# Kernel tuning notes

Hardware: AMD Instinct MI355X
Metric: run time of the kernel (lower is better)

## Reference

```python
import jax, jax.numpy as jnp
import numpy as np

B, IN, ED, PW, OUT, CL, NK = 2048, 4096, 8192, 2048, 256, 16, 32
MIX = 0.5

def _onehot_mask(key, n):
    # near-one-hot selector matrix [n, NK], as built by forward_update_masks
    idx = jax.random.choice(key, n, (NK,), replace=False)
    return jnp.zeros((n, NK), jnp.float32).at[idx, jnp.arange(NK)].set(1.0)

def setup_inputs():
    ks = jax.random.split(jax.random.key(0), 24)
    f = jnp.float32
    adj = (jax.random.uniform(ks[4], (IN, IN)) < 0.01).astype(f)
    adj = jnp.maximum(adj, adj.T).at[jnp.arange(IN), jnp.arange(IN)].set(1.0)
    return {
        'x_gene': jax.random.normal(ks[0], (B, IN), f),
        'x_invmea': jax.random.normal(ks[1], (B, IN), f),
        'x_curv': jax.random.normal(ks[2], (B, ED), f),
        'clinn': jax.random.normal(ks[3], (B, CL), f),
        'Adj': adj,
        'edge_mask': (jax.random.uniform(ks[5], (ED, IN)) < 0.005).astype(f),
        'pathway_mask': (jax.random.uniform(ks[6], (PW, ED)) < 0.02).astype(f),
        'top_gene_mask': _onehot_mask(ks[7], IN),
        'top_invmea_mask': _onehot_mask(ks[8], IN),
        'top_curv_mask': _onehot_mask(ks[9], ED),
        'top_path_mask': _onehot_mask(ks[10], PW),
        'W1': jnp.full((IN, IN), 0.05, f),
        'b1': 0.01 * jax.random.normal(ks[11], (IN,), f),
        'W2': jnp.full((ED, IN), 0.05, f),
        'b2': 0.01 * jax.random.normal(ks[12], (ED,), f),
        'W3': jnp.full((PW, ED), 0.05, f),
        'b3': 0.01 * jax.random.normal(ks[13], (PW,), f),
        'W4': 0.02 * jax.random.normal(ks[14], (OUT, PW), f),
        'b4': 0.01 * jax.random.normal(ks[15], (OUT,), f),
        'W5': 0.02 * jax.random.normal(ks[16], (OUT, OUT), f),
        'b5': 0.01 * jax.random.normal(ks[17], (OUT,), f),
        'W6': 0.05 * jax.random.normal(ks[18], (OUT, OUT + CL + 4 * NK), f),
        'W7': 0.05 * jax.random.normal(ks[19], (1, OUT), f),
        'mp11': MIX * jnp.ones(IN, f),
        'mp12': (1.0 - MIX) * jnp.ones(IN, f),
        'mp1': jnp.ones(IN, f),
        'mp21': MIX * jnp.ones(ED, f),
        'mp22': (1.0 - MIX) * jnp.ones(ED, f),
        'mp2': jnp.ones(ED, f),
        'mp3': jnp.ones(PW, f),
    }

def reference(x_gene, x_invmea, x_curv, clinn, Adj, edge_mask, pathway_mask,
              top_gene_mask, top_invmea_mask, top_curv_mask, top_path_mask,
              W1, b1, W2, b2, W3, b3, W4, b4, W5, b5, W6, W7,
              mp11, mp12, mp1, mp21, mp22, mp2, mp3):
    sg = jax.lax.stop_gradient
    sig = jax.nn.sigmoid
    kept_gene = sg(x_gene @ top_gene_mask)                     # [B,NK] gather-as-matmul
    x1 = sig(x_gene @ (W1 * Adj).T + b1)                       # masked linear [B,IN]
    x1 = x_invmea * (mp11 * mp1) + x1 * (mp12 * mp1)
    kept_invmea = sg(x1 @ top_invmea_mask)
    x1 = sig(x1 @ (W2 * edge_mask).T + b2)                     # [B,ED]
    x1 = x_curv * (mp21 * mp2) + x1 * (mp22 * mp2)
    kept_curv = sg(x1 @ top_curv_mask)
    x1 = sig(x1 @ (W3 * pathway_mask).T + b3)                  # [B,PW]
    x1 = x1 * mp3
    kept_path = sg(x1 @ top_path_mask)
    x1 = sig(x1 @ W4.T + b4)
    x1 = sig(x1 @ W5.T + b5)                                   # [B,OUT]
    x_cat = jnp.concatenate([x1, kept_gene, kept_invmea, kept_curv, kept_path, clinn], axis=1)
    lp = sig(x_cat @ W6.T)
    lp = lp - jnp.mean(lp, axis=1, keepdims=True)
    return lp @ W7.T                                           # [B,1]
```

## Files before the change

kernel.cpp:

```cpp
#include <hip/hip_runtime.h>

typedef unsigned short u16;
typedef __attribute__((ext_vector_type(4))) float f32x4;
typedef __attribute__((ext_vector_type(8))) short s16x8;

__device__ __forceinline__ u16 f2bf(float f) {
    union { float f; unsigned u; } c; c.f = f;
    return (u16)((c.u + 0x7fffu + ((c.u >> 16) & 1u)) >> 16);
}
__device__ __forceinline__ float bf2f(u16 u) {
    union { unsigned u; float f; } c; c.u = ((unsigned)u) << 16; return c.f;
}
__device__ __forceinline__ unsigned pk2(float a, float b) {
    return (unsigned)f2bf(a) | ((unsigned)f2bf(b) << 16);
}
__device__ __forceinline__ float sigm(float x) { return 1.0f / (1.0f + __expf(-x)); }
__device__ __forceinline__ void fma2(unsigned xv, float w, float& a0, float& a1) {
    union { float f; unsigned u; } lo, hi;
    lo.u = xv << 16; hi.u = xv & 0xFFFF0000u;
    a0 += w * lo.f; a1 += w * hi.f;
}

__device__ __forceinline__ void load16_g2l(const void* g, void* l) {
    __builtin_amdgcn_global_load_lds(
        (const __attribute__((address_space(1))) unsigned int*)(unsigned long long)g,
        (__attribute__((address_space(3))) unsigned int*)(unsigned int)(unsigned long long)l,
        16, 0, 0);
}

#define GSTR 2112

__device__ void d_transpF(const float* __restrict__ in, u16* __restrict__ out,
                          int ldo, int Cc, int bx, int by, float (*t)[65]) {
    const int r0 = by * 64, c0 = bx * 64;
    const int tid = threadIdx.x;
#pragma unroll
    for (int i = 0; i < 4; i++) {
        int idx = tid + i * 256;
        int rr = idx >> 4, c4 = (idx & 15) * 4;
        float4 v = *(const float4*)(in + (size_t)(r0 + rr) * Cc + c0 + c4);
        t[rr][c4 + 0] = v.x; t[rr][c4 + 1] = v.y;
        t[rr][c4 + 2] = v.z; t[rr][c4 + 3] = v.w;
    }
    __syncthreads();
#pragma unroll
    for (int i = 0; i < 8; i++) {
        int idx = tid + i * 256;
        int cc = idx >> 5, rp = (idx & 31) * 2;
        unsigned p = pk2(t[rp][cc], t[rp + 1][cc]);
        *(unsigned*)(out + (size_t)(c0 + cc) * ldo + r0 + rp) = p;
    }
}

__device__ void d_find(const float* __restrict__ mask, int n, int* __restrict__ outp,
                       int* red, int k) {
    int best = -1;
    for (int i = threadIdx.x; i < n; i += 256)
        if (mask[(size_t)i * 32 + k] != 0.0f) best = i;
    red[threadIdx.x] = best;
    __syncthreads();
    for (int off = 128; off > 0; off >>= 1) {
        if (threadIdx.x < off) {
            int o = red[threadIdx.x + off];
            if (o > red[threadIdx.x]) red[threadIdx.x] = o;
        }
        __syncthreads();
    }
    if (threadIdx.x == 0) *outp = red[0] < 0 ? 0 : red[0];
}

__device__ void d_conv(const float* __restrict__ in, u16* __restrict__ out,
                       int bid, unsigned n8) {
    unsigned i = bid * 256u + threadIdx.x;
    if (i >= n8) return;
    float4 a = ((const float4*)in)[2 * i];
    float4 b = ((const float4*)in)[2 * i + 1];
    uint4 o;
    o.x = pk2(a.x, a.y); o.y = pk2(a.z, a.w);
    o.z = pk2(b.x, b.y); o.w = pk2(b.z, b.w);
    ((uint4*)out)[i] = o;
}

template <int SUBC>
__device__ void d_ell_row(const float* __restrict__ M, const float* __restrict__ W,
                          unsigned* __restrict__ ell, int* __restrict__ cnt,
                          int PAD, int row, int* __restrict__ lds) {
    const int lane = threadIdx.x & 63;
    const int wv = threadIdx.x >> 6;
    const int C = SUBC * 4096;
    const float4* mrow = (const float4*)(M + (size_t)row * C);
    const float4* wrow = (const float4*)(W + (size_t)row * C);
    unsigned* erow = ell + (size_t)row * PAD;

    float4 m[SUBC * 4];
#pragma unroll
    for (int k = 0; k < SUBC * 4; k++) {
        int sc = k >> 2, i = k & 3;
        m[k] = mrow[(wv * SUBC + sc) * 256 + lane + i * 64];
    }
    unsigned bits[SUBC];
    int total = 0;
#pragma unroll
    for (int sc = 0; sc < SUBC; sc++) {
        unsigned b = 0;
#pragma unroll
        for (int i = 0; i < 4; i++) {
            const float4 mm = m[sc * 4 + i];
            if (mm.x != 0.f) b |= 1u << (4 * i);
            if (mm.y != 0.f) b |= 2u << (4 * i);
            if (mm.z != 0.f) b |= 4u << (4 * i);
            if (mm.w != 0.f) b |= 8u << (4 * i);
        }
        bits[sc] = b;
        total += __popc(b);
    }
    float4 w[SUBC * 4];
#pragma unroll
    for (int k = 0; k < SUBC * 4; k++) {
        int sc = k >> 2, i = k & 3;
        if ((bits[sc] >> (4 * i)) & 0xFu)
            w[k] = wrow[(wv * SUBC + sc) * 256 + lane + i * 64];
    }
    int pre = total;
#pragma unroll
    for (int off = 1; off < 64; off <<= 1) {
        int t = __shfl_up(pre, off, 64);
        if (lane >= off) pre += t;
    }
    if (lane == 63) lds[wv] = pre;
    __syncthreads();
    int base = 0;
#pragma unroll
    for (int v = 0; v < 3; v++) if (v < wv) base += lds[v];
    int s = base + pre - total;
    __asm__ volatile("" ::: "memory");
#pragma unroll
    for (int sc = 0; sc < SUBC; sc++) {
        const unsigned b = bits[sc];
        const int f4b = (wv * SUBC + sc) * 256;
#pragma unroll
        for (int i = 0; i < 4; i++) {
            if ((b >> (4 * i)) & 0xFu) {
                const float4 wv4 = w[sc * 4 + i];
                int c = (f4b + lane + i * 64) * 4;
                if (b & (1u << (4 * i))) { if (s < PAD) erow[s] = ((unsigned)f2bf(wv4.x) << 16) | (unsigned)(c + 0); s++; }
                if (b & (2u << (4 * i))) { if (s < PAD) erow[s] = ((unsigned)f2bf(wv4.y) << 16) | (unsigned)(c + 1); s++; }
                if (b & (4u << (4 * i))) { if (s < PAD) erow[s] = ((unsigned)f2bf(wv4.z) << 16) | (unsigned)(c + 2); s++; }
                if (b & (8u << (4 * i))) { if (s < PAD) erow[s] = ((unsigned)f2bf(wv4.w) << 16) | (unsigned)(c + 3); s++; }
            }
        }
    }
    if (threadIdx.x == 0) {
        int rt = lds[0] + lds[1] + lds[2] + lds[3];
        cnt[row] = rt > PAD ? PAD : rt;
    }
}

__global__ __launch_bounds__(256) void prep_part(
    int ebase, int ecount, int mbase, int mcount,
    const float* __restrict__ Adj, const float* __restrict__ W1,
    unsigned* __restrict__ ell1, int* __restrict__ cnt1,
    const float* __restrict__ edge, const float* __restrict__ W2,
    unsigned* __restrict__ ell2, int* __restrict__ cnt2,
    const float* __restrict__ path, const float* __restrict__ W3,
    unsigned* __restrict__ ell3, int* __restrict__ cnt3,
    const float* __restrict__ xg_f, const float* __restrict__ xinv_f,
    const float* __restrict__ xcv_f,
    u16* __restrict__ xTg, u16* __restrict__ xinvT, u16* __restrict__ xcvT,
    const float* __restrict__ m0, const float* __restrict__ m1,
    const float* __restrict__ m2, const float* __restrict__ m3,
    int* __restrict__ idx,
    const float* __restrict__ W4, u16* __restrict__ w4b,
    const float* __restrict__ W5, u16* __restrict__ w5b) {
    __shared__ float tile[64][65];
    const long long T = ecount + mcount, E = ecount;
    const int b = blockIdx.x;
    const int ea = (int)(((long long)b * E) / T);
    const int eb2 = (int)(((long long)(b + 1) * E) / T);
    if (eb2 > ea) {
        int id = ebase + ea;
        if (id < 4096) { d_ell_row<1>(Adj, W1, ell1, cnt1, 256, id, (int*)tile); return; }
        id -= 4096;
        if (id < 8192) { d_ell_row<1>(edge, W2, ell2, cnt2, 96, id, (int*)tile); return; }
        d_ell_row<2>(path, W3, ell3, cnt3, 320, id - 8192, (int*)tile);
        return;
    }
    int id = mbase + (b - ea);
    if (id < 2048) { d_transpF(xg_f, xTg, GSTR, 4096, id & 63, id >> 6, tile); return; }
    id -= 2048;
    if (id < 2048) { d_transpF(xinv_f, xinvT, 2048, 4096, id & 63, id >> 6, tile); return; }
    id -= 2048;
    if (id < 4096) { d_transpF(xcv_f, xcvT, 2048, 8192, id & 127, id >> 7, tile); return; }
    id -= 4096;
    if (id < 128) {
        const float* mk; int n;
        int which = id >> 5;
        if (which == 0)      { mk = m0; n = 4096; }
        else if (which == 1) { mk = m1; n = 4096; }
        else if (which == 2) { mk = m2; n = 8192; }
        else                 { mk = m3; n = 2048; }
        d_find(mk, n, idx + which * 32 + (id & 31), (int*)tile, id & 31);
        return;
    }
    id -= 128;
    if (id < 256) { d_conv(W4, w4b, id, 65536u); return; }
    id -= 256;
    d_conv(W5, w5b, id, 8192u);
}

template <int BPL, int LAYER, int XSTR, int ISTR, int OSTR>
__global__ __launch_bounds__(256) void spmm(const unsigned* __restrict__ ell,
                                            const int* __restrict__ cnt,
                                            const u16* __restrict__ xT,
                                            u16* __restrict__ outT,
                                            const float* __restrict__ bias,
                                            const float* __restrict__ c1a,
                                            const float* __restrict__ c1b,
                                            const float* __restrict__ c2a,
                                            const float* __restrict__ c2b,
                                            const u16* __restrict__ invT,
                                            const int* __restrict__ gidx,
                                            u16* __restrict__ gdst,
                                            int PAD) {
    const int lane = threadIdx.x & 63;
    const int wv = __builtin_amdgcn_readfirstlane((int)(threadIdx.x >> 6));
    const int j = blockIdx.x * 4 + wv;
    const int b0 = blockIdx.y * (64 * BPL) + lane * BPL;

    const unsigned* ep = ell + (size_t)j * PAD;
    int len = cnt[j];
    if (len > PAD) len = PAD;

    float acc[BPL];
#pragma unroll
    for (int i = 0; i < BPL; i++) acc[i] = 0.f;

    const int nfull = len >> 3;
    unsigned eA[8];
    if (nfull > 0) {
#pragma unroll
        for (int t = 0; t < 8; t++) eA[t] = ep[t];
    }
    for (int g = 0; g < nfull; g++) {
        unsigned eB[8];
        const bool more = (g + 1 < nfull);
        if (more) {
#pragma unroll
            for (int t = 0; t < 8; t++) eB[t] = ep[(g + 1) * 8 + t];
        }
        uint2 xv[8];
#pragma unroll
        for (int t = 0; t < 8; t++)
            xv[t] = *(const uint2*)(xT + (size_t)(eA[t] & 0xFFFFu) * XSTR + b0);
#pragma unroll
        for (int t = 0; t < 8; t++) {
            union { float f; unsigned u; } w; w.u = (eA[t] >> 16) << 16;
            fma2(xv[t].x, w.f, acc[0], acc[1]);
            fma2(xv[t].y, w.f, acc[2], acc[3]);
        }
        if (more) {
#pragma unroll
            for (int t = 0; t < 8; t++) eA[t] = eB[t];
        }
    }
    for (int s = nfull * 8; s < len; ++s) {
        unsigned e = ep[s];
        union { float f; unsigned u; } w; w.u = (e >> 16) << 16;
        const u16* xp = xT + (size_t)(e & 0xFFFFu) * XSTR + b0;
        uint2 xv = *(const uint2*)xp;
        fma2(xv.x, w.f, acc[0], acc[1]); fma2(xv.y, w.f, acc[2], acc[3]);
    }

    const float bi = bias[j];
    float c1 = 0.f;
    if (c1a) { c1 = c1a[j]; if (c1b) c1 *= c1b[j]; }
    float c2 = 1.f;
    if (c2a) { c2 = c2a[j]; if (c2b) c2 *= c2b[j]; }

    float v[BPL];
#pragma unroll
    for (int i = 0; i < BPL; i++) v[i] = sigm(acc[i] + bi) * c2;
    if (invT) {
        const unsigned long long* ip = (const unsigned long long*)(invT + (size_t)j * ISTR + b0);
#pragma unroll
        for (int h = 0; h < BPL / 4; h++) {
            unsigned long long iv = __builtin_nontemporal_load(ip + h);
            unsigned lo = (unsigned)iv, hi = (unsigned)(iv >> 32);
            union { float f; unsigned u; } g0, g1, g2, g3;
            g0.u = lo << 16; g1.u = lo & 0xFFFF0000u;
            g2.u = hi << 16; g3.u = hi & 0xFFFF0000u;
            v[4 * h + 0] += g0.f * c1; v[4 * h + 1] += g1.f * c1;
            v[4 * h + 2] += g2.f * c1; v[4 * h + 3] += g3.f * c1;
        }
    }
    unsigned long long pkv[BPL / 4];
#pragma unroll
    for (int h = 0; h < BPL / 4; h++)
        pkv[h] = (unsigned long long)pk2(v[4 * h + 0], v[4 * h + 1])
               | ((unsigned long long)pk2(v[4 * h + 2], v[4 * h + 3]) << 32);
    unsigned long long* op = (unsigned long long*)(outT + (size_t)j * OSTR + b0);
#pragma unroll
    for (int h = 0; h < BPL / 4; h++) __builtin_nontemporal_store(pkv[h], op + h);

    if (gdst) {
        for (int t = 0; t < 32; t++) {
            if (gidx[t] == j) {
                unsigned long long* gp = (unsigned long long*)(gdst + t * 2048 + b0);
#pragma unroll
                for (int h = 0; h < BPL / 4; h++) gp[h] = pkv[h];
            }
        }
    }
}

template <int XSTR>
__global__ __launch_bounds__(256) void spmm_ph(const unsigned* __restrict__ ell,
                                               const int* __restrict__ cnt,
                                               const u16* __restrict__ xT,
                                               u16* __restrict__ outT,
                                               const float* __restrict__ bias,
                                               const float* __restrict__ scale,
                                               const int* __restrict__ gidx,
                                               u16* __restrict__ gdst,
                                               int PAD) {
    const int lane = threadIdx.x & 63;
    const int wv = __builtin_amdgcn_readfirstlane((int)(threadIdx.x >> 6));
    const int j = blockIdx.x * 4 + wv;
    const int b0 = blockIdx.y * 128 + lane * 2;

    const unsigned* ep = ell + (size_t)j * PAD;
    int len = cnt[j];
    if (len > PAD) len = PAD;

    float a0 = 0.f, a1 = 0.f;
    const int nfull = len >> 4;
    unsigned eA[16];
    if (nfull > 0) {
#pragma unroll
        for (int t = 0; t < 16; t++) eA[t] = ep[t];
    }
    for (int g = 0; g < nfull; g++) {
        unsigned eB[16];
        const bool more = (g + 1 < nfull);
        if (more) {
#pragma unroll
            for (int t = 0; t < 16; t++) eB[t] = ep[(g + 1) * 16 + t];
        }
        unsigned xv[16];
#pragma unroll
        for (int t = 0; t < 16; t++)
            xv[t] = *(const unsigned*)(xT + (size_t)(eA[t] & 0xFFFFu) * XSTR + b0);
#pragma unroll
        for (int t = 0; t < 16; t++) {
            union { float f; unsigned u; } w; w.u = (eA[t] >> 16) << 16;
            fma2(xv[t], w.f, a0, a1);
        }
        if (more) {
#pragma unroll
            for (int t = 0; t < 16; t++) eA[t] = eB[t];
        }
    }
    for (int s = nfull * 16; s < len; ++s) {
        unsigned e = ep[s];
        union { float f; unsigned u; } w; w.u = (e >> 16) << 16;
        unsigned xv = *(const unsigned*)(xT + (size_t)(e & 0xFFFFu) * XSTR + b0);
        fma2(xv, w.f, a0, a1);
    }

    const float bi = bias[j];
    const float sc = scale[j];
    const unsigned pk = pk2(sigm(a0 + bi) * sc, sigm(a1 + bi) * sc);
    *(unsigned*)(outT + ((size_t)j << 11) + b0) = pk;

    if (gdst) {
        for (int t = 0; t < 32; t++) {
            if (gidx[t] == j)
                *(unsigned*)(gdst + t * 2048 + b0) = pk;
        }
    }
}

__global__ __launch_bounds__(256) void gatherFT(const float* __restrict__ src, int ld,
                                                const int* __restrict__ idx,
                                                u16* __restrict__ dstT) {
    int i = blockIdx.x * 256 + threadIdx.x;
    int kk = i >> 11, b = i & 2047;
    dstT[i] = f2bf(src[(size_t)b * ld + idx[kk]]);
}

__global__ __launch_bounds__(256) void transpB(const u16* __restrict__ in,
                                               u16* __restrict__ out, int Rr, int Cc) {
    __shared__ u16 t[64][66];
    const int r0 = blockIdx.y * 64, c0 = blockIdx.x * 64;
    const int tid = threadIdx.x;
#pragma unroll
    for (int i = 0; i < 16; i++) {
        int idx = tid + i * 256;
        int rr = idx >> 6, cc = idx & 63;
        t[rr][cc] = in[(size_t)(r0 + rr) * Cc + c0 + cc];
    }
    __syncthreads();
#pragma unroll
    for (int i = 0; i < 16; i++) {
        int idx = tid + i * 256;
        int cc = idx >> 6, rr = idx & 63;
        out[(size_t)(c0 + cc) * Rr + r0 + rr] = t[rr][cc];
    }
}

template <int WR, int WC, int MF, int NF, int KC, int WPE>
__global__ __launch_bounds__(WR * WC * 64, WPE)
void gemm_t(const u16* __restrict__ A, const u16* __restrict__ W,
            u16* __restrict__ Out, const float* __restrict__ bias, int N, int K) {
    constexpr int NTHR = WR * WC * 64;
    constexpr int BM = WR * MF * 16;
    constexpr int BN = WC * NF * 16;
    constexpr int BK = KC * 32;
    constexpr int CPR = KC * 4;
    constexpr int MSK = CPR - 1;
    constexpr int CA = BM * CPR / NTHR;
    constexpr int CB = BN * CPR / NTHR;
    constexpr int L  = CA + CB;

    __shared__ u16 At[2][BM * BK];
    __shared__ u16 Bt[2][BN * BK];

    const int tid = threadIdx.x;
    const int lane = tid & 63;
    const int wave = tid >> 6;
    const int wr = wave / WC, wc = wave % WC;
    const int tn = blockIdx.x, tm = blockIdx.y;
    const int r16 = lane & 15;
    const int q = lane >> 4;

    const u16* aSrc[CA]; int aDst[CA];
#pragma unroll
    for (int j = 0; j < CA; j++) {
        int c = tid + j * NTHR;
        int r = c / CPR, p = c - r * CPR;
        aSrc[j] = A + (size_t)(tm * BM + r) * K + (p ^ (r & MSK)) * 8;
        aDst[j] = c * 8;
    }
    const u16* bSrc[CB]; int bDst[CB];
#pragma unroll
    for (int j = 0; j < CB; j++) {
        int c = tid + j * NTHR;
        int r = c / CPR, p = c - r * CPR;
        bSrc[j] = W + (size_t)(tn * BN + r) * K + (p ^ (r & MSK)) * 8;
        bDst[j] = c * 8;
    }
    int aRd[MF][KC], bRd[NF][KC];
#pragma unroll
    for (int mi = 0; mi < MF; mi++)
#pragma unroll
        for (int kc = 0; kc < KC; kc++)
            aRd[mi][kc] = (wr * MF * 16 + mi * 16 + r16) * BK + (((kc * 4 + q) ^ (r16 & MSK)) << 3);
#pragma unroll
    for (int ni = 0; ni < NF; ni++)
#pragma unroll
        for (int kc = 0; kc < KC; kc++)
            bRd[ni][kc] = (wc * NF * 16 + ni * 16 + r16) * BK + (((kc * 4 + q) ^ (r16 & MSK)) << 3);

    const int nIter = K / BK;

#define ISSUE(slot, it_)                                              \
    do {                                                              \
        const int k0_ = (it_) * BK;                                   \
        _Pragma("unroll")                                             \
        for (int j = 0; j < CA; j++)                                  \
            load16_g2l(aSrc[j] + k0_, &At[slot][aDst[j]]);            \
        _Pragma("unroll")                                             \
        for (int j = 0; j < CB; j++)                                  \
            load16_g2l(bSrc[j] + k0_, &Bt[slot][bDst[j]]);            \
    } while (0)

    ISSUE(0, 0);
    if (nIter > 1) ISSUE(1, 1);

    f32x4 acc[MF][NF];
#pragma unroll
    for (int i = 0; i < MF; i++)
#pragma unroll
        for (int j = 0; j < NF; j++) acc[i][j] = (f32x4){0.f, 0.f, 0.f, 0.f};

    for (int it = 0; it < nIter; ++it) {
        const int s = it & 1;
        if (it + 1 < nIter) __builtin_amdgcn_s_waitcnt(0xF70 | L);
        else                __builtin_amdgcn_s_waitcnt(0xF70);
        __asm__ volatile("" ::: "memory");
        __builtin_amdgcn_s_barrier();
        __asm__ volatile("" ::: "memory");

        s16x8 af[KC][MF], bfr[KC][NF];
#pragma unroll
        for (int kc = 0; kc < KC; kc++) {
#pragma unroll
            for (int mi = 0; mi < MF; mi++) af[kc][mi] = *(const s16x8*)(&At[s][aRd[mi][kc]]);
#pragma unroll
            for (int ni = 0; ni < NF; ni++) bfr[kc][ni] = *(const s16x8*)(&Bt[s][bRd[ni][kc]]);
        }
        __asm__ volatile("" ::: "memory");
        __builtin_amdgcn_s_waitcnt(0xC07F);
        __builtin_amdgcn_s_barrier();
        __asm__ volatile("" ::: "memory");

        if (it + 2 < nIter) ISSUE(s, it + 2);

#pragma unroll
        for (int kc = 0; kc < KC; kc++)
#pragma unroll
            for (int mi = 0; mi < MF; mi++)
#pragma unroll
                for (int ni = 0; ni < NF; ni++)
                    acc[mi][ni] = __builtin_amdgcn_mfma_f32_16x16x32_bf16(af[kc][mi], bfr[kc][ni], acc[mi][ni], 0, 0, 0);
    }
#undef ISSUE

#pragma unroll
    for (int ni = 0; ni < NF; ni++) {
        const int n = tn * BN + wc * NF * 16 + ni * 16 + r16;
        const float bi = bias ? bias[n] : 0.f;
#pragma unroll
        for (int mi = 0; mi < MF; mi++) {
#pragma unroll
            for (int rg = 0; rg < 4; rg++) {
                const int m = tm * BM + wr * MF * 16 + mi * 16 + q * 4 + rg;
                Out[(size_t)m * N + n] = f2bf(sigm(acc[mi][ni][rg] + bi));
            }
        }
    }
}

__global__ __launch_bounds__(256) void tail_k(const u16* __restrict__ x5,
                                              const u16* __restrict__ kgT,
                                              const u16* __restrict__ kiT,
                                              const u16* __restrict__ kcT,
                                              const u16* __restrict__ kpT,
                                              const float* __restrict__ clinn,
                                              const float* __restrict__ W6,
                                              const float* __restrict__ W7,
                                              float* __restrict__ out) {
    __shared__ float xs[8 * 400];
    __shared__ float s1[4][8], s2[4][8], s3[4];
    const int tid = threadIdx.x;
    const int b0 = blockIdx.x * 8;
    for (int i = tid; i < 8 * 400; i += 256) {
        int r = i / 400, c = i - r * 400;
        int b = b0 + r;
        float v;
        if (c < 256)      v = bf2f(x5[b * 256 + c]);
        else if (c < 288) v = bf2f(kgT[(c - 256) * 2048 + b]);
        else if (c < 320) v = bf2f(kiT[(c - 288) * 2048 + b]);
        else if (c < 352) v = bf2f(kcT[(c - 320) * 2048 + b]);
        else if (c < 384) v = bf2f(kpT[(c - 352) * 2048 + b]);
        else              v = clinn[b * 16 + (c - 384)];
        xs[i] = v;
    }
    __syncthreads();
    const int j = tid;
    float acc[8];
#pragma unroll
    for (int r = 0; r < 8; r++) acc[r] = 0.f;
    const float4* wrow = (const float4*)(W6 + (size_t)j * 400);
    for (int c = 0; c < 100; c++) {
        float4 wv = wrow[c];
        const float* wp = (const float*)&wv;
#pragma unroll
        for (int t = 0; t < 4; t++) {
            float w = wp[t];
            int k = c * 4 + t;
#pragma unroll
            for (int r = 0; r < 8; r++) acc[r] += w * xs[r * 400 + k];
        }
    }
    const float w7j = W7[j];
    const int lane = tid & 63, wave = tid >> 6;
    float t3 = w7j;
#pragma unroll
    for (int off = 32; off > 0; off >>= 1) t3 += __shfl_down(t3, off, 64);
    if (lane == 0) s3[wave] = t3;
#pragma unroll
    for (int r = 0; r < 8; r++) {
        float lp = sigm(acc[r]);
        float t1 = lp, t2 = lp * w7j;
#pragma unroll
        for (int off = 32; off > 0; off >>= 1) {
            t1 += __shfl_down(t1, off, 64);
            t2 += __shfl_down(t2, off, 64);
        }
        if (lane == 0) { s1[wave][r] = t1; s2[wave][r] = t2; }
    }
    __syncthreads();
    if (tid < 8) {
        float S1 = s1[0][tid] + s1[1][tid] + s1[2][tid] + s1[3][tid];
        float S2 = s2[0][tid] + s2[1][tid] + s2[2][tid] + s2[3][tid];
        float SW = s3[0] + s3[1] + s3[2] + s3[3];
        out[b0 + tid] = S2 - (S1 * (1.f / 256.f)) * SW;
    }
}

extern "C" void kernel_launch(void* const* d_in, const int* in_sizes, int n_in,
                              void* d_out, int out_size, void* d_ws, size_t ws_size,
                              hipStream_t stream) {
    const float* x_gene   = (const float*)d_in[0];
    const float* x_invmea = (const float*)d_in[1];
    const float* x_curv   = (const float*)d_in[2];
    const float* clinn    = (const float*)d_in[3];
    const float* Adj      = (const float*)d_in[4];
    const float* edge_m   = (const float*)d_in[5];
    const float* path_m   = (const float*)d_in[6];
    const float* tg_mask  = (const float*)d_in[7];
    const float* ti_mask  = (const float*)d_in[8];
    const float* tc_mask  = (const float*)d_in[9];
    const float* tp_mask  = (const float*)d_in[10];
    const float* W1 = (const float*)d_in[11];  const float* b1 = (const float*)d_in[12];
    const float* W2 = (const float*)d_in[13];  const float* b2 = (const float*)d_in[14];
    const float* W3 = (const float*)d_in[15];  const float* b3 = (const float*)d_in[16];
    const float* W4 = (const float*)d_in[17];  const float* b4 = (const float*)d_in[18];
    const float* W5 = (const float*)d_in[19];  const float* b5 = (const float*)d_in[20];
    const float* W6 = (const float*)d_in[21];
    const float* W7 = (const float*)d_in[22];
    const float* mp11 = (const float*)d_in[23];
    const float* mp12 = (const float*)d_in[24];
    const float* mp1  = (const float*)d_in[25];
    const float* mp21 = (const float*)d_in[26];
    const float* mp22 = (const float*)d_in[27];
    const float* mp2  = (const float*)d_in[28];
    const float* mp3  = (const float*)d_in[29];

    char* ws = (char*)d_ws;
    const float* nulf = nullptr;
    float* out = (float*)d_out;

    u16*  xTg   = (u16*)(ws + 0);
    u16*  x3T   = (u16*)(ws + 0);
    u16*  xinvT = (u16*)(ws + 17301504);
    u16*  xcvT  = (u16*)(ws + 34078720);
    u16*  x1T   = (u16*)(ws + 67633152);
    u16*  x2T   = (u16*)(ws + 84934656);
    u16*  x3    = (u16*)(ws + 119537664);
    unsigned* ell1 = (unsigned*)(ws + 127926272);
    unsigned* ell2 = (unsigned*)(ws + 132120576);
    unsigned* ell3 = (unsigned*)(ws + 135266304);
    int* cnt1 = (int*)(ws + 137887744);
    int* cnt2 = (int*)(ws + 137904128);
    int* cnt3 = (int*)(ws + 137936896);
    int* idxg = (int*)(ws + 137953280);
    int* idxi = idxg + 32;
    int* idxc = idxg + 64;
    int* idxp = idxg + 96;
    u16* kgT  = (u16*)(ws + 137957376);
    u16* kiT  = (u16*)(ws + 138088448);
    u16* kcT  = (u16*)(ws + 138219520);
    u16* kpT  = (u16*)(ws + 138350592);
    u16* w4b  = (u16*)(ws + 138481664);
    u16* w5b  = (u16*)(ws + 139530240);
    u16* x4   = (u16*)(ws + 139661312);
    u16* x5   = (u16*)(ws + 140709888);

    prep_part<<<11472, 256, 0, stream>>>(
        0, 7168, 0, 4304,
        Adj, W1, ell1, cnt1, edge_m, W2, ell2, cnt2, path_m, W3, ell3, cnt3,
        x_gene, x_invmea, x_curv, xTg, xinvT, xcvT,
        tg_mask, ti_mask, tc_mask, tp_mask, idxg, W4, w4b, W5, w5b);
    prep_part<<<11472, 256, 0, stream>>>(
        7168, 7168, 4304, 4304,
        Adj, W1, ell1, cnt1, edge_m, W2, ell2, cnt2, path_m, W3, ell3, cnt3,
        x_gene, x_invmea, x_curv, xTg, xinvT, xcvT,
        tg_mask, ti_mask, tc_mask, tp_mask, idxg, W4, w4b, W5, w5b);
    gatherFT<<<256, 256, 0, stream>>>(x_gene, 4096, idxg, kgT);

    spmm<4, 1, GSTR, 2048, GSTR><<<dim3(1024, 8), 256, 0, stream>>>(
        ell1, cnt1, xTg, x1T, b1, mp11, mp1, mp12, mp1, xinvT, idxi, kiT, 256);
    spmm<4, 2, GSTR, 2048, GSTR><<<dim3(2048, 8), 256, 0, stream>>>(
        ell2, cnt2, x1T, x2T, b2, mp21, mp2, mp22, mp2, xcvT, idxc, kcT, 96);
    spmm_ph<GSTR><<<dim3(512, 16), 256, 0, stream>>>(ell3, cnt3, x2T, x3T, b3,
                                                     mp3, idxp, kpT, 320);
    transpB<<<dim3(32, 32), 256, 0, stream>>>(x3T, x3, 2048, 2048);

    gemm_t<2, 2, 2, 2, 2, 4><<<dim3(4, 32), 256, 0, stream>>>(x3, w4b, x4, b4, 256, 2048);
    gemm_t<2, 2, 2, 2, 2, 4><<<dim3(4, 32), 256, 0, stream>>>(x4, w5b, x5, b5, 256, 256);

    tail_k<<<256, 256, 0, stream>>>(x5, kgT, kiT, kcT, kpT, clinn, W6, W7, out);
}
```

Baseline: 859.1 us.

## Use packed FMA in SpMM, single-pass mask index search, unpadded gather stride

The SpMM inner loops now accumulate into two-wide float vectors through elementwise FMA, which should let the compiler emit packed FMA instructions. The top-k mask index search scans each mask row once per block with float4 loads and LDS atomicMax over all 32 columns, replacing 32 strided single-column scans. The prep launch shrinks to match the fewer find blocks. The transposed-activation row stride drops from padded 2112 to 2048, which may bring back LDS or cache channel conflicts that the padding was there to avoid.

```diff
diff --git a/kernel.cpp b/kernel.cpp
--- a/kernel.cpp
+++ b/kernel.cpp
@@ -2,6 +2,7 @@
 
 typedef unsigned short u16;
 typedef __attribute__((ext_vector_type(4))) float f32x4;
+typedef __attribute__((ext_vector_type(2))) float f32x2;
 typedef __attribute__((ext_vector_type(8))) short s16x8;
 
 __device__ __forceinline__ u16 f2bf(float f) {
@@ -15,10 +16,12 @@
     return (unsigned)f2bf(a) | ((unsigned)f2bf(b) << 16);
 }
 __device__ __forceinline__ float sigm(float x) { return 1.0f / (1.0f + __expf(-x)); }
-__device__ __forceinline__ void fma2(unsigned xv, float w, float& a0, float& a1) {
+
+__device__ __forceinline__ void fma2v(unsigned xv, f32x2 wp, f32x2& a) {
     union { float f; unsigned u; } lo, hi;
     lo.u = xv << 16; hi.u = xv & 0xFFFF0000u;
-    a0 += w * lo.f; a1 += w * hi.f;
+    f32x2 xp = {lo.f, hi.f};
+    a = __builtin_elementwise_fma(xp, wp, a);
 }
 
 __device__ __forceinline__ void load16_g2l(const void* g, void* l) {
@@ -28,7 +31,7 @@
         16, 0, 0);
 }
 
-#define GSTR 2112
+#define GSTR 2048
 
 __device__ void d_transpF(const float* __restrict__ in, u16* __restrict__ out,
                           int ldo, int Cc, int bx, int by, float (*t)[65]) {
@@ -52,21 +55,24 @@
     }
 }
 
-__device__ void d_find(const float* __restrict__ mask, int n, int* __restrict__ outp,
-                       int* red, int k) {
-    int best = -1;
-    for (int i = threadIdx.x; i < n; i += 256)
-        if (mask[(size_t)i * 32 + k] != 0.0f) best = i;
-    red[threadIdx.x] = best;
+__device__ void d_find32(const float* __restrict__ mask, int n,
+                         int* __restrict__ outp, int* fidx) {
+    const int tid = threadIdx.x;
+    if (tid < 32) fidx[tid] = 0;
     __syncthreads();
-    for (int off = 128; off > 0; off >>= 1) {
-        if (threadIdx.x < off) {
-            int o = red[threadIdx.x + off];
-            if (o > red[threadIdx.x]) red[threadIdx.x] = o;
-        }
-        __syncthreads();
-    }
-    if (threadIdx.x == 0) *outp = red[0] < 0 ? 0 : red[0];
+    for (int i = tid; i < n; i += 256) {
+        const float4* row = (const float4*)(mask + (size_t)i * 32);
+#pragma unroll
+        for (int q = 0; q < 8; q++) {
+            float4 v = row[q];
+            if (v.x != 0.f) atomicMax(&fidx[q * 4 + 0], i);
+            if (v.y != 0.f) atomicMax(&fidx[q * 4 + 1], i);
+            if (v.z != 0.f) atomicMax(&fidx[q * 4 + 2], i);
+            if (v.w != 0.f) atomicMax(&fidx[q * 4 + 3], i);
+        }
+    }
+    __syncthreads();
+    if (tid < 32) outp[tid] = fidx[tid];
 }
 
 __device__ void d_conv(const float* __restrict__ in, u16* __restrict__ out,
@@ -192,17 +198,16 @@
     id -= 2048;
     if (id < 4096) { d_transpF(xcv_f, xcvT, 2048, 8192, id & 127, id >> 7, tile); return; }
     id -= 4096;
-    if (id < 128) {
+    if (id < 4) {
         const float* mk; int n;
-        int which = id >> 5;
-        if (which == 0)      { mk = m0; n = 4096; }
-        else if (which == 1) { mk = m1; n = 4096; }
-        else if (which == 2) { mk = m2; n = 8192; }
-        else                 { mk = m3; n = 2048; }
-        d_find(mk, n, idx + which * 32 + (id & 31), (int*)tile, id & 31);
+        if (id == 0)      { mk = m0; n = 4096; }
+        else if (id == 1) { mk = m1; n = 4096; }
+        else if (id == 2) { mk = m2; n = 8192; }
+        else              { mk = m3; n = 2048; }
+        d_find32(mk, n, idx + id * 32, (int*)tile);
         return;
     }
-    id -= 128;
+    id -= 4;
     if (id < 256) { d_conv(W4, w4b, id, 65536u); return; }
     id -= 256;
     d_conv(W5, w5b, id, 8192u);
@@ -231,9 +236,9 @@
     int len = cnt[j];
     if (len > PAD) len = PAD;
 
-    float acc[BPL];
-#pragma unroll
-    for (int i = 0; i < BPL; i++) acc[i] = 0.f;
+    f32x2 acc2[BPL / 2];
+#pragma unroll
+    for (int i = 0; i < BPL / 2; i++) acc2[i] = (f32x2){0.f, 0.f};
 
     const int nfull = len >> 3;
     unsigned eA[8];
@@ -255,8 +260,9 @@
 #pragma unroll
         for (int t = 0; t < 8; t++) {
             union { float f; unsigned u; } w; w.u = (eA[t] >> 16) << 16;
-            fma2(xv[t].x, w.f, acc[0], acc[1]);
-            fma2(xv[t].y, w.f, acc[2], acc[3]);
+            f32x2 wp = {w.f, w.f};
+            fma2v(xv[t].x, wp, acc2[0]);
+            fma2v(xv[t].y, wp, acc2[1]);
         }
         if (more) {
 #pragma unroll
@@ -266,10 +272,15 @@
     for (int s = nfull * 8; s < len; ++s) {
         unsigned e = ep[s];
         union { float f; unsigned u; } w; w.u = (e >> 16) << 16;
+        f32x2 wp = {w.f, w.f};
         const u16* xp = xT + (size_t)(e & 0xFFFFu) * XSTR + b0;
         uint2 xv = *(const uint2*)xp;
-        fma2(xv.x, w.f, acc[0], acc[1]); fma2(xv.y, w.f, acc[2], acc[3]);
-    }
+        fma2v(xv.x, wp, acc2[0]); fma2v(xv.y, wp, acc2[1]);
+    }
+
+    float acc[BPL];
+#pragma unroll
+    for (int i = 0; i < BPL / 2; i++) { acc[2 * i] = acc2[i].x; acc[2 * i + 1] = acc2[i].y; }
 
     const float bi = bias[j];
     float c1 = 0.f;
@@ -332,7 +343,7 @@
     int len = cnt[j];
     if (len > PAD) len = PAD;
 
-    float a0 = 0.f, a1 = 0.f;
+    f32x2 a2 = (f32x2){0.f, 0.f};
     const int nfull = len >> 4;
     unsigned eA[16];
     if (nfull > 0) {
@@ -353,7 +364,8 @@
 #pragma unroll
         for (int t = 0; t < 16; t++) {
             union { float f; unsigned u; } w; w.u = (eA[t] >> 16) << 16;
-            fma2(xv[t], w.f, a0, a1);
+            f32x2 wp = {w.f, w.f};
+            fma2v(xv[t], wp, a2);
         }
         if (more) {
 #pragma unroll
@@ -363,13 +375,14 @@
     for (int s = nfull * 16; s < len; ++s) {
         unsigned e = ep[s];
         union { float f; unsigned u; } w; w.u = (e >> 16) << 16;
+        f32x2 wp = {w.f, w.f};
         unsigned xv = *(const unsigned*)(xT + (size_t)(e & 0xFFFFu) * XSTR + b0);
-        fma2(xv, w.f, a0, a1);
+        fma2v(xv, wp, a2);
     }
 
     const float bi = bias[j];
     const float sc = scale[j];
-    const unsigned pk = pk2(sigm(a0 + bi) * sc, sigm(a1 + bi) * sc);
+    const unsigned pk = pk2(sigm(a2.x + bi) * sc, sigm(a2.y + bi) * sc);
     *(unsigned*)(outT + ((size_t)j << 11) + b0) = pk;
 
     if (gdst) {
@@ -658,13 +671,13 @@
     u16* x4   = (u16*)(ws + 139661312);
     u16* x5   = (u16*)(ws + 140709888);
 
-    prep_part<<<11472, 256, 0, stream>>>(
-        0, 7168, 0, 4304,
+    prep_part<<<11410, 256, 0, stream>>>(
+        0, 7168, 0, 4242,
         Adj, W1, ell1, cnt1, edge_m, W2, ell2, cnt2, path_m, W3, ell3, cnt3,
         x_gene, x_invmea, x_curv, xTg, xinvT, xcvT,
         tg_mask, ti_mask, tc_mask, tp_mask, idxg, W4, w4b, W5, w5b);
-    prep_part<<<11472, 256, 0, stream>>>(
-        7168, 7168, 4304, 4304,
+    prep_part<<<11410, 256, 0, stream>>>(
+        7168, 7168, 4242, 4242,
         Adj, W1, ell1, cnt1, edge_m, W2, ell2, cnt2, path_m, W3, ell3, cnt3,
         x_gene, x_invmea, x_curv, xTg, xinvT, xcvT,
         tg_mask, ti_mask, tc_mask, tp_mask, idxg, W4, w4b, W5, w5b);
```

Result: slower. 926.5 us (+7.8%).
